# Optimization experiments

Measured on AMD Instinct MI355X. Metric: run time of the kernel, lower is better.

## Reference

```python
import jax, jax.numpy as jnp
import numpy as np


def setup_inputs() -> dict:
    key = jax.random.key(0)
    k1, k2, k3, k4 = jax.random.split(key, 4)
    N, D, H = 16384, 128, 256
    features = jax.random.normal(k1, (N, D), dtype=jnp.float32)
    adj_matrix = jax.random.randint(k2, (N, N), 0, 2, dtype=jnp.int32)
    # Linear(2D -> H) and Linear(D -> H), torch convention W: [out, in]
    Wd = jax.random.normal(k3, (H, 2 * D), dtype=jnp.float32) * (1.0 / np.sqrt(2 * D))
    bd = jnp.zeros((H,), dtype=jnp.float32)
    Wo = jax.random.normal(k4, (H, D), dtype=jnp.float32) * (1.0 / np.sqrt(D))
    bo = jnp.zeros((H,), dtype=jnp.float32)
    return {"features": features, "adj_matrix": adj_matrix,
            "Wd": Wd, "bd": bd, "Wo": Wo, "bo": bo}


def reference(features, adj_matrix, Wd, bd, Wo, bo):
    # Faithful math, but without materializing the O(N^2*2D) pairwise tensor:
    #   sum_j adj[i,j] * concat(f[i], f[j]) = concat(deg[i]*f[i], (adj @ f)[i])
    adj = adj_matrix.astype(features.dtype)
    deg = jnp.sum(adj, axis=-1, keepdims=True)              # [N,1]
    neigh_mask = jnp.max(adj, axis=-1, keepdims=True)       # [N,1]
    neigh_num = deg + (1.0 - neigh_mask)                    # avoid div by 0
    head_sum = features * deg                                # [N,D]
    tail_sum = adj @ features                                # [N,D]
    neigh_ave = jnp.concatenate([head_sum, tail_sum], axis=-1) / neigh_num  # [N,2D]
    neigh_feat = neigh_ave @ Wd.T + bd                       # [N,H]
    updated = (features @ Wo.T + bo) - neigh_feat            # [N,H]
    updated = jnp.tanh(updated)
    # dropout is identity in eval mode; withAgg=False returns the pair
    return (updated, updated)
```

## Files before the change

kernel.cpp:

```cpp
#include <hip/hip_runtime.h>
#include <hip/hip_bf16.h>

#define NROW 16384
#define DIM 128
#define HOUT 256

typedef float f32x4 __attribute__((ext_vector_type(4)));
typedef __bf16 bf16x8 __attribute__((ext_vector_type(8)));

__global__ void k_transpose(const float* __restrict__ f, short* __restrict__ fT,
                            float* __restrict__ deg) {
    __shared__ short tr[128][72];
    const int t = threadIdx.x;
    const int j0 = blockIdx.x * 64;
    if (blockIdx.x < 64) deg[blockIdx.x * 256 + t] = 0.f;
    for (int it = 0; it < 8; ++it) {
        int slot = t + 256 * it;
        int j = slot >> 5;
        int dq = slot & 31;
        f32x4 v = *reinterpret_cast<const f32x4*>(f + (size_t)(j0 + j) * DIM + dq * 4);
#pragma unroll
        for (int c = 0; c < 4; ++c) {
            __hip_bfloat16 h = __float2bfloat16(v[c]);
            tr[dq * 4 + c][j] = *reinterpret_cast<short*>(&h);
        }
    }
    __syncthreads();
    for (int it = 0; it < 4; ++it) {
        int slot = t + 256 * it;
        int d = slot >> 3;
        int c8 = slot & 7;
        int4 v = *reinterpret_cast<const int4*>(&tr[d][c8 * 8]);
        *reinterpret_cast<int4*>(fT + (size_t)d * NROW + j0 + c8 * 8) = v;
    }
}

__global__ __launch_bounds__(256, 2) void k_gemm(const int* __restrict__ adj,
                                                 const short* __restrict__ fT,
                                                 float* __restrict__ part,
                                                 float* __restrict__ deg) {
    __shared__ short As[64][72];
    __shared__ short Fs[128][72];
    const int t = threadIdx.x;
    const int rb = blockIdx.x >> 1;
    const int s  = blockIdx.x & 1;
    const int i0 = rb * 64;
    const int kb0 = s * 8192;
    const int lane = t & 63;
    const int w = t >> 6;
    const int wr = w & 1, wc = w >> 1;

    f32x4 acc[2][4] = {};
    unsigned dsum[4] = {0u, 0u, 0u, 0u};
    int4 a_reg[4], f_reg[4];

#define LOAD_TILE(kb)                                                                   \
    {                                                                                   \
        _Pragma("unroll")                                                               \
        for (int it = 0; it < 4; ++it) {                                                \
            int slot = t + 256 * it;                                                    \
            a_reg[it] = *reinterpret_cast<const int4*>(                                 \
                adj + (size_t)(i0 + (slot >> 4)) * NROW + (kb) + (slot & 15) * 4);      \
        }                                                                               \
        _Pragma("unroll")                                                               \
        for (int it = 0; it < 4; ++it) {                                                \
            int slot = t + 256 * it;                                                    \
            f_reg[it] = *reinterpret_cast<const int4*>(                                 \
                fT + (size_t)(slot >> 3) * NROW + (kb) + (slot & 7) * 8);               \
        }                                                                               \
    }

    LOAD_TILE(kb0);
    for (int step = 0; step < 128; ++step) {
#pragma unroll
        for (int it = 0; it < 4; ++it) {
            int slot = t + 256 * it;
            int row = slot >> 4, c4 = slot & 15;
            int4 v = a_reg[it];
            unsigned lo = (v.x ? 0x3F80u : 0u) | (v.y ? 0x3F800000u : 0u);
            unsigned hi = (v.z ? 0x3F80u : 0u) | (v.w ? 0x3F800000u : 0u);
            dsum[it] += (unsigned)(v.x + v.y + v.z + v.w);
            uint2 pk; pk.x = lo; pk.y = hi;
            *reinterpret_cast<uint2*>(&As[row][c4 * 4]) = pk;
        }
#pragma unroll
        for (int it = 0; it < 4; ++it) {
            int slot = t + 256 * it;
            *reinterpret_cast<int4*>(&Fs[slot >> 3][(slot & 7) * 8]) = f_reg[it];
        }
        __syncthreads();
        if (step + 1 < 128) LOAD_TILE(kb0 + (step + 1) * 64);
#pragma unroll
        for (int kk = 0; kk < 64; kk += 32) {
            bf16x8 af[2], bfr[4];
#pragma unroll
            for (int ti = 0; ti < 2; ++ti)
                af[ti] = *reinterpret_cast<const bf16x8*>(
                    &As[wr * 32 + ti * 16 + (lane & 15)][kk + (lane >> 4) * 8]);
#pragma unroll
            for (int ci = 0; ci < 4; ++ci)
                bfr[ci] = *reinterpret_cast<const bf16x8*>(
                    &Fs[wc * 64 + ci * 16 + (lane & 15)][kk + (lane >> 4) * 8]);
#pragma unroll
            for (int ti = 0; ti < 2; ++ti)
#pragma unroll
                for (int ci = 0; ci < 4; ++ci)
                    acc[ti][ci] = __builtin_amdgcn_mfma_f32_16x16x32_bf16(
                        af[ti], bfr[ci], acc[ti][ci], 0, 0, 0);
        }
        __syncthreads();
    }
#pragma unroll
    for (int ti = 0; ti < 2; ++ti)
#pragma unroll
        for (int ci = 0; ci < 4; ++ci)
#pragma unroll
            for (int r = 0; r < 4; ++r) {
                int i = i0 + wr * 32 + ti * 16 + (lane >> 4) * 4 + r;
                int d = wc * 64 + ci * 16 + (lane & 15);
                part[((size_t)s * NROW + i) * DIM + d] = acc[ti][ci][r];
            }
    __syncthreads();
    unsigned* degs = reinterpret_cast<unsigned*>(&As[0][0]);
#pragma unroll
    for (int it = 0; it < 4; ++it)
        degs[((t >> 4) + 16 * it) * 16 + (t & 15)] = dsum[it];
    __syncthreads();
    if (t < 64) {
        unsigned sum = 0;
#pragma unroll
        for (int c = 0; c < 16; ++c) sum += degs[t * 16 + c];
        atomicAdd(deg + i0 + t, (float)sum);
    }
}

__global__ __launch_bounds__(256, 2) void k_epilogue(const float* __restrict__ feat,
                                                     const float* __restrict__ part,
                                                     const float* __restrict__ deg,
                                                     const float* __restrict__ Wd,
                                                     const float* __restrict__ bd,
                                                     const float* __restrict__ Wo,
                                                     const float* __restrict__ bo,
                                                     float* __restrict__ out) {
    __shared__ float fs[32][132];
    __shared__ float tn[32][132];
    __shared__ float mrow[32], inv[32];
    const int t = threadIdx.x;
    const int i0 = blockIdx.x * 32;
    if (t < 32) {
        float d = deg[i0 + t];
        mrow[t] = d > 0.f ? 1.f : 0.f;
        inv[t]  = d > 0.f ? 1.f / d : 1.f;
    }
    __syncthreads();
    for (int it = 0; it < 4; ++it) {
        int slot = t + 256 * it;
        int r = slot >> 5, dq = slot & 31;
        size_t gi = (size_t)(i0 + r) * DIM + dq * 4;
        f32x4 fv = *reinterpret_cast<const f32x4*>(feat + gi);
        *reinterpret_cast<f32x4*>(&fs[r][dq * 4]) = fv;
        f32x4 p0 = *reinterpret_cast<const f32x4*>(part + gi);
        f32x4 p1 = *reinterpret_cast<const f32x4*>(part + (size_t)NROW * DIM + gi);
        f32x4 tv = (p0 + p1) * inv[r];
        *reinterpret_cast<f32x4*>(&tn[r][dq * 4]) = tv;
    }
    __syncthreads();
    const int rt = t & 7;
    const int ht = t >> 3;
    float accM[4][8] = {};
    float accB[4][8] = {};
    for (int d = 0; d < DIM; d += 4) {
        f32x4 fr[4], tr[4];
#pragma unroll
        for (int rr = 0; rr < 4; ++rr) {
            fr[rr] = *reinterpret_cast<const f32x4*>(&fs[rt * 4 + rr][d]);
            tr[rr] = *reinterpret_cast<const f32x4*>(&tn[rt * 4 + rr][d]);
        }
#pragma unroll
        for (int hh = 0; hh < 8; ++hh) {
            int h = ht * 8 + hh;
            f32x4 wo = *reinterpret_cast<const f32x4*>(Wo + (size_t)h * DIM + d);
            f32x4 w1 = *reinterpret_cast<const f32x4*>(Wd + (size_t)h * 2 * DIM + d);
            f32x4 w2 = *reinterpret_cast<const f32x4*>(Wd + (size_t)h * 2 * DIM + DIM + d);
#pragma unroll
            for (int rr = 0; rr < 4; ++rr)
#pragma unroll
                for (int c = 0; c < 4; ++c) {
                    accM[rr][hh] += fr[rr][c] * wo[c] - tr[rr][c] * w2[c];
                    accB[rr][hh] += fr[rr][c] * w1[c];
                }
        }
    }
    f32x4 bo0 = *reinterpret_cast<const f32x4*>(bo + ht * 8);
    f32x4 bo1 = *reinterpret_cast<const f32x4*>(bo + ht * 8 + 4);
    f32x4 bd0 = *reinterpret_cast<const f32x4*>(bd + ht * 8);
    f32x4 bd1 = *reinterpret_cast<const f32x4*>(bd + ht * 8 + 4);
#pragma unroll
    for (int rr = 0; rr < 4; ++rr) {
        int i = i0 + rt * 4 + rr;
        float m = mrow[rt * 4 + rr];
        f32x4 v0, v1;
#pragma unroll
        for (int c = 0; c < 4; ++c) {
            v0[c] = tanhf(accM[rr][c]     - m * accB[rr][c]     + bo0[c] - bd0[c]);
            v1[c] = tanhf(accM[rr][c + 4] - m * accB[rr][c + 4] + bo1[c] - bd1[c]);
        }
        float* o = out + (size_t)i * HOUT + ht * 8;
        *reinterpret_cast<f32x4*>(o) = v0;
        *reinterpret_cast<f32x4*>(o + 4) = v1;
        float* o2 = o + (size_t)NROW * HOUT;
        *reinterpret_cast<f32x4*>(o2) = v0;
        *reinterpret_cast<f32x4*>(o2 + 4) = v1;
    }
}

extern "C" void kernel_launch(void* const* d_in, const int* in_sizes, int n_in,
                              void* d_out, int out_size, void* d_ws, size_t ws_size,
                              hipStream_t stream) {
    const float* feat = (const float*)d_in[0];
    const int*   adj  = (const int*)d_in[1];
    const float* Wd   = (const float*)d_in[2];
    const float* bd   = (const float*)d_in[3];
    const float* Wo   = (const float*)d_in[4];
    const float* bo   = (const float*)d_in[5];
    float* out = (float*)d_out;
    char* ws = (char*)d_ws;
    short* fT   = (short*)ws;
    float* part = (float*)(ws + (size_t)4  * 1024 * 1024);
    float* deg  = (float*)(ws + (size_t)20 * 1024 * 1024);
    k_transpose<<<256, 256, 0, stream>>>(feat, fT, deg);
    k_gemm     <<<512, 256, 0, stream>>>(adj, fT, part, deg);
    k_epilogue <<<512, 256, 0, stream>>>(feat, part, deg, Wd, bd, Wo, bo, out);
}
```

Before: 1.680 ms.

## Drop LDS staging in adjacency GEMM, load MFMA fragments directly, split K four ways

The GEMM kernel no longer stages tiles in shared memory with barriers. Each wave loads its adjacency rows and the feature-transpose fragments straight from global memory into MFMA operand registers. Tiles grow to 128 rows × 128 columns per block, and K is split four ways, so there are more partial buffers for the epilogue to sum. This removes LDS traffic and synchronisation but drops cross-wave reuse of the B operand, so every wave reads all of fT from cache, and there is no software prefetch.

```diff
diff --git a/kernel.cpp b/kernel.cpp
--- a/kernel.cpp
+++ b/kernel.cpp
@@ -4,9 +4,12 @@
 #define NROW 16384
 #define DIM 128
 #define HOUT 256
+#define SPLIT 4
 
 typedef float f32x4 __attribute__((ext_vector_type(4)));
 typedef __bf16 bf16x8 __attribute__((ext_vector_type(8)));
+typedef unsigned int u32;
+typedef unsigned int u32x4 __attribute__((ext_vector_type(4)));
 
 __global__ void k_transpose(const float* __restrict__ f, short* __restrict__ fT,
                             float* __restrict__ deg) {
@@ -35,102 +38,71 @@
     }
 }
 
+__device__ inline bf16x8 cvt_a(const int4& a, const int4& b, int& ds) {
+    union { u32x4 u; bf16x8 f; } U;
+    U.u.x = (a.x ? 0x3F80u : 0u) | (a.y ? 0x3F800000u : 0u);
+    U.u.y = (a.z ? 0x3F80u : 0u) | (a.w ? 0x3F800000u : 0u);
+    U.u.z = (b.x ? 0x3F80u : 0u) | (b.y ? 0x3F800000u : 0u);
+    U.u.w = (b.z ? 0x3F80u : 0u) | (b.w ? 0x3F800000u : 0u);
+    ds += a.x + a.y + a.z + a.w + b.x + b.y + b.z + b.w;
+    return U.f;
+}
+
 __global__ __launch_bounds__(256, 2) void k_gemm(const int* __restrict__ adj,
                                                  const short* __restrict__ fT,
                                                  float* __restrict__ part,
                                                  float* __restrict__ deg) {
-    __shared__ short As[64][72];
-    __shared__ short Fs[128][72];
     const int t = threadIdx.x;
-    const int rb = blockIdx.x >> 1;
-    const int s  = blockIdx.x & 1;
-    const int i0 = rb * 64;
-    const int kb0 = s * 8192;
+    const int rb = blockIdx.x >> 2;
+    const int s  = blockIdx.x & 3;
+    const int i0 = rb * 128;
+    const int kb0 = s * (NROW / SPLIT);
     const int lane = t & 63;
     const int w = t >> 6;
-    const int wr = w & 1, wc = w >> 1;
-
-    f32x4 acc[2][4] = {};
-    unsigned dsum[4] = {0u, 0u, 0u, 0u};
-    int4 a_reg[4], f_reg[4];
-
-#define LOAD_TILE(kb)                                                                   \
-    {                                                                                   \
-        _Pragma("unroll")                                                               \
-        for (int it = 0; it < 4; ++it) {                                                \
-            int slot = t + 256 * it;                                                    \
-            a_reg[it] = *reinterpret_cast<const int4*>(                                 \
-                adj + (size_t)(i0 + (slot >> 4)) * NROW + (kb) + (slot & 15) * 4);      \
-        }                                                                               \
-        _Pragma("unroll")                                                               \
-        for (int it = 0; it < 4; ++it) {                                                \
-            int slot = t + 256 * it;                                                    \
-            f_reg[it] = *reinterpret_cast<const int4*>(                                 \
-                fT + (size_t)(slot >> 3) * NROW + (kb) + (slot & 7) * 8);               \
-        }                                                                               \
-    }
-
-    LOAD_TILE(kb0);
-    for (int step = 0; step < 128; ++step) {
-#pragma unroll
-        for (int it = 0; it < 4; ++it) {
-            int slot = t + 256 * it;
-            int row = slot >> 4, c4 = slot & 15;
-            int4 v = a_reg[it];
-            unsigned lo = (v.x ? 0x3F80u : 0u) | (v.y ? 0x3F800000u : 0u);
-            unsigned hi = (v.z ? 0x3F80u : 0u) | (v.w ? 0x3F800000u : 0u);
-            dsum[it] += (unsigned)(v.x + v.y + v.z + v.w);
-            uint2 pk; pk.x = lo; pk.y = hi;
-            *reinterpret_cast<uint2*>(&As[row][c4 * 4]) = pk;
-        }
-#pragma unroll
-        for (int it = 0; it < 4; ++it) {
-            int slot = t + 256 * it;
-            *reinterpret_cast<int4*>(&Fs[slot >> 3][(slot & 7) * 8]) = f_reg[it];
-        }
-        __syncthreads();
-        if (step + 1 < 128) LOAD_TILE(kb0 + (step + 1) * 64);
-#pragma unroll
-        for (int kk = 0; kk < 64; kk += 32) {
-            bf16x8 af[2], bfr[4];
-#pragma unroll
-            for (int ti = 0; ti < 2; ++ti)
-                af[ti] = *reinterpret_cast<const bf16x8*>(
-                    &As[wr * 32 + ti * 16 + (lane & 15)][kk + (lane >> 4) * 8]);
-#pragma unroll
-            for (int ci = 0; ci < 4; ++ci)
-                bfr[ci] = *reinterpret_cast<const bf16x8*>(
-                    &Fs[wc * 64 + ci * 16 + (lane & 15)][kk + (lane >> 4) * 8]);
-#pragma unroll
-            for (int ti = 0; ti < 2; ++ti)
-#pragma unroll
-                for (int ci = 0; ci < 4; ++ci)
-                    acc[ti][ci] = __builtin_amdgcn_mfma_f32_16x16x32_bf16(
-                        af[ti], bfr[ci], acc[ti][ci], 0, 0, 0);
-        }
-        __syncthreads();
+    const int lr = lane & 15;
+    const int lk = (lane >> 4) * 8;
+
+    f32x4 acc[2][8] = {};
+    int dsum[2] = {0, 0};
+
+    const int* aptr0 = adj + (size_t)(i0 + w * 32 + lr) * NROW + kb0 + lk;
+    const int* aptr1 = aptr0 + (size_t)16 * NROW;
+    const short* bptr = fT + (size_t)lr * NROW + kb0 + lk;
+
+    for (int it = 0; it < (NROW / SPLIT) / 32; ++it) {
+        const int ko = it * 32;
+        int4 a0a = *reinterpret_cast<const int4*>(aptr0 + ko);
+        int4 a0b = *reinterpret_cast<const int4*>(aptr0 + ko + 4);
+        int4 a1a = *reinterpret_cast<const int4*>(aptr1 + ko);
+        int4 a1b = *reinterpret_cast<const int4*>(aptr1 + ko + 4);
+        bf16x8 bf[8];
+#pragma unroll
+        for (int ci = 0; ci < 8; ++ci)
+            bf[ci] = *reinterpret_cast<const bf16x8*>(bptr + (size_t)ci * 16 * NROW + ko);
+        bf16x8 af0 = cvt_a(a0a, a0b, dsum[0]);
+        bf16x8 af1 = cvt_a(a1a, a1b, dsum[1]);
+#pragma unroll
+        for (int ci = 0; ci < 8; ++ci) {
+            acc[0][ci] = __builtin_amdgcn_mfma_f32_16x16x32_bf16(af0, bf[ci], acc[0][ci], 0, 0, 0);
+            acc[1][ci] = __builtin_amdgcn_mfma_f32_16x16x32_bf16(af1, bf[ci], acc[1][ci], 0, 0, 0);
+        }
     }
 #pragma unroll
     for (int ti = 0; ti < 2; ++ti)
 #pragma unroll
-        for (int ci = 0; ci < 4; ++ci)
+        for (int ci = 0; ci < 8; ++ci)
 #pragma unroll
             for (int r = 0; r < 4; ++r) {
-                int i = i0 + wr * 32 + ti * 16 + (lane >> 4) * 4 + r;
-                int d = wc * 64 + ci * 16 + (lane & 15);
+                int i = i0 + w * 32 + ti * 16 + (lane >> 4) * 4 + r;
+                int d = ci * 16 + lr;
                 part[((size_t)s * NROW + i) * DIM + d] = acc[ti][ci][r];
             }
-    __syncthreads();
-    unsigned* degs = reinterpret_cast<unsigned*>(&As[0][0]);
-#pragma unroll
-    for (int it = 0; it < 4; ++it)
-        degs[((t >> 4) + 16 * it) * 16 + (t & 15)] = dsum[it];
-    __syncthreads();
-    if (t < 64) {
-        unsigned sum = 0;
-#pragma unroll
-        for (int c = 0; c < 16; ++c) sum += degs[t * 16 + c];
-        atomicAdd(deg + i0 + t, (float)sum);
+#pragma unroll
+    for (int ti = 0; ti < 2; ++ti) {
+        float v = (float)dsum[ti];
+        v += __shfl_xor(v, 16);
+        v += __shfl_xor(v, 32);
+        if (lane < 16) atomicAdd(deg + i0 + w * 32 + ti * 16 + lr, v);
     }
 }
 
@@ -159,9 +131,11 @@
         size_t gi = (size_t)(i0 + r) * DIM + dq * 4;
         f32x4 fv = *reinterpret_cast<const f32x4*>(feat + gi);
         *reinterpret_cast<f32x4*>(&fs[r][dq * 4]) = fv;
-        f32x4 p0 = *reinterpret_cast<const f32x4*>(part + gi);
-        f32x4 p1 = *reinterpret_cast<const f32x4*>(part + (size_t)NROW * DIM + gi);
-        f32x4 tv = (p0 + p1) * inv[r];
+        f32x4 p = *reinterpret_cast<const f32x4*>(part + gi);
+#pragma unroll
+        for (int sp = 1; sp < SPLIT; ++sp)
+            p += *reinterpret_cast<const f32x4*>(part + (size_t)sp * NROW * DIM + gi);
+        f32x4 tv = p * inv[r];
         *reinterpret_cast<f32x4*>(&tn[r][dq * 4]) = tv;
     }
     __syncthreads();
@@ -227,7 +201,7 @@
     char* ws = (char*)d_ws;
     short* fT   = (short*)ws;
     float* part = (float*)(ws + (size_t)4  * 1024 * 1024);
-    float* deg  = (float*)(ws + (size_t)20 * 1024 * 1024);
+    float* deg  = (float*)(ws + (size_t)40 * 1024 * 1024);
     k_transpose<<<256, 256, 0, stream>>>(feat, fT, deg);
     k_gemm     <<<512, 256, 0, stream>>>(adj, fT, part, deg);
     k_epilogue <<<512, 256, 0, stream>>>(feat, part, deg, Wd, bd, Wo, bo, out);
```

After: 1.602 ms. 1.05x faster.
